# Optimization experiments

Measured on AMD Instinct MI355X. Metric: run time of the kernel, lower is better.

## Reference

```python
import jax, jax.numpy as jnp
import numpy as np
import math

B, S, D = 4, 2048, 768
H = 12
DH = D // H  # 64
NEG = -1e10

def setup_inputs() -> dict:
    key = jax.random.key(0)
    ks = jax.random.split(key, 8)
    scale = 0.02
    return {
        "hidden_states": jax.random.normal(ks[0], (B, S, D), dtype=jnp.float32),
        "attention_mask": jnp.zeros((B, 1, 1, S), dtype=jnp.float32),
        "Wq": jax.random.normal(ks[1], (D, D), dtype=jnp.float32) * scale,
        "bq": jnp.zeros((D,), dtype=jnp.float32),
        "Wk": jax.random.normal(ks[2], (D, D), dtype=jnp.float32) * scale,
        "bk": jnp.zeros((D,), dtype=jnp.float32),
        "Wv": jax.random.normal(ks[3], (D, D), dtype=jnp.float32) * scale,
        "bv": jnp.zeros((D,), dtype=jnp.float32),
    }

def reference(hidden_states, attention_mask, Wq, bq, Wk, bk, Wv, bv):
    # Linear projections; note attention_mask is accepted but unused, matching the torch module.
    def split_heads(x):  # [B,S,D] -> [B,H,S,DH]
        return x.reshape(B, S, H, DH).transpose(0, 2, 1, 3)
    q = split_heads(hidden_states @ Wq + bq)
    k = split_heads(hidden_states @ Wk + bk)
    v = split_heads(hidden_states @ Wv + bv)
    scores = jnp.einsum("bhqd,bhkd->bhqk", q, k) / math.sqrt(DH)
    causal = jnp.tril(jnp.ones((S, S), dtype=bool))  # masked_fill(mask==0, -1e10)
    scores = jnp.where(causal, scores, NEG)
    probs = jax.nn.softmax(scores, axis=-1)
    # dropout prob = 0.0 (eval) -> identity
    ctx = jnp.einsum("bhqk,bhkd->bhqd", probs, v)
    return ctx.transpose(0, 2, 1, 3).reshape(B, S, D)
```

## Files before the change

kernel.cpp:

```cpp
#include <hip/hip_runtime.h>
#include <hip/hip_bf16.h>

#define B_  4
#define S_  2048
#define D_  768
#define H_  12
#define DH_ 64

typedef __bf16 bf16;
typedef __attribute__((ext_vector_type(8))) __bf16 bf16x8;
typedef __attribute__((ext_vector_type(4))) __bf16 bf16x4;
typedef __attribute__((ext_vector_type(4))) float floatx4;
typedef __attribute__((ext_vector_type(16))) float floatx16;

__device__ __forceinline__ void load_lds16(const bf16* g, bf16* l) {
    __builtin_amdgcn_global_load_lds((const __attribute__((address_space(1))) void*)g,
                                     (__attribute__((address_space(3))) void*)l, 16, 0, 0);
}

__device__ __forceinline__ unsigned pack2(float a, float b) {
    unsigned ua = __builtin_bit_cast(unsigned, a) + 0x8000u;
    unsigned ub = __builtin_bit_cast(unsigned, b) + 0x8000u;
    return __builtin_amdgcn_perm(ub, ua, 0x07060302);
}

__device__ __forceinline__ int chunk_off2(int qt2) {
    if (qt2 < 4)  return qt2;
    if (qt2 < 8)  return 4 + 2 * (qt2 - 4);
    if (qt2 < 12) return 12 + 3 * (qt2 - 8);
    return 24 + 4 * (qt2 - 12);
}

__global__ __launch_bounds__(256) void cvt_f32_bf16(const float* __restrict__ in,
                                                    bf16* __restrict__ out, int n4) {
    int i = blockIdx.x * 256 + threadIdx.x;
    if (i < n4) {
        float4 v = ((const float4*)in)[i];
        bf16x4 o;
        o[0] = (bf16)v.x; o[1] = (bf16)v.y; o[2] = (bf16)v.z; o[3] = (bf16)v.w;
        *(bf16x4*)(out + (size_t)i * 4) = o;
    }
}

__global__ __launch_bounds__(256) void w_transpose(const float* __restrict__ w0,
                                                   const float* __restrict__ w1,
                                                   const float* __restrict__ w2,
                                                   bf16* __restrict__ Wt)
{
    const int which = blockIdx.z;
    const float* W = (which == 0) ? w0 : (which == 1 ? w1 : w2);
    bf16* dst = Wt + (size_t)which * D_ * D_;
    __shared__ bf16 t[64 * 72];
    const int k0 = blockIdx.x * 64, n0 = blockIdx.y * 64;
    const int tid = threadIdx.x;
    {
        int r = tid >> 2;
        int c0 = (tid & 3) * 16;
        #pragma unroll
        for (int q = 0; q < 4; q++) {
            float4 v = *(const float4*)(W + (size_t)(k0 + r) * D_ + n0 + c0 + q * 4);
            t[(c0 + q * 4 + 0) * 72 + r] = (bf16)v.x;
            t[(c0 + q * 4 + 1) * 72 + r] = (bf16)v.y;
            t[(c0 + q * 4 + 2) * 72 + r] = (bf16)v.z;
            t[(c0 + q * 4 + 3) * 72 + r] = (bf16)v.w;
        }
    }
    __syncthreads();
    {
        int n = tid >> 3, seg = tid & 7;
        *(bf16x8*)(dst + (size_t)(n0 + n) * D_ + k0 + seg * 8) =
            *(const bf16x8*)(t + n * 72 + seg * 8);
        *(bf16x8*)(dst + (size_t)(n0 + n + 32) * D_ + k0 + seg * 8) =
            *(const bf16x8*)(t + (n + 32) * 72 + seg * 8);
    }
}

__global__ __launch_bounds__(256) void qkv_gemm(
    const bf16* __restrict__ Xb, const bf16* __restrict__ Wt,
    const float* __restrict__ bq, const float* __restrict__ bk,
    const float* __restrict__ bv, bf16* __restrict__ QKV)
{
    const int which = blockIdx.z;
    const bf16* Wm = Wt + (size_t)which * D_ * D_;
    const float* bias = (which == 0) ? bq : (which == 1 ? bk : bv);
    bf16* out = QKV + (size_t)which * B_ * H_ * S_ * DH_;

    __shared__ bf16 As[128 * 64];
    __shared__ bf16 Bs[128 * 64];

    const int tid  = threadIdx.x;
    const int wave = tid >> 6, lane = tid & 63;
    const int wr = wave >> 1, wc = wave & 1;
    const int g = lane >> 4, ln = lane & 15;
    const int m0 = blockIdx.x * 128, n0 = blockIdx.y * 128;
    const int fbase = wave * 256 + lane;

    floatx4 acc[4][4];
    #pragma unroll
    for (int i = 0; i < 4; i++)
        #pragma unroll
        for (int j = 0; j < 4; j++)
            acc[i][j] = (floatx4){0.f, 0.f, 0.f, 0.f};

    for (int k0 = 0; k0 < D_; k0 += 64) {
        __syncthreads();
        #pragma unroll
        for (int i = 0; i < 4; i++) {
            int fc = fbase + i * 64;
            int row = fc >> 3;
            int seg = (fc & 7) ^ (row & 7);
            load_lds16(Xb + (size_t)(m0 + row) * D_ + k0 + seg * 8, As + fc * 8);
            load_lds16(Wm + (size_t)(n0 + row) * D_ + k0 + seg * 8, Bs + fc * 8);
        }
        __syncthreads();
        #pragma unroll
        for (int ks = 0; ks < 2; ks++) {
            const int sx = ((ks * 4 + g) ^ (ln & 7)) * 8;
            bf16x8 af[4], bfr[4];
            #pragma unroll
            for (int i = 0; i < 4; i++)
                af[i] = *(const bf16x8*)(As + ((wr * 64 + i * 16 + ln) << 6) + sx);
            #pragma unroll
            for (int j = 0; j < 4; j++)
                bfr[j] = *(const bf16x8*)(Bs + ((wc * 64 + j * 16 + ln) << 6) + sx);
            #pragma unroll
            for (int i = 0; i < 4; i++)
                #pragma unroll
                for (int j = 0; j < 4; j++)
                    acc[i][j] = __builtin_amdgcn_mfma_f32_16x16x32_bf16(af[i], bfr[j], acc[i][j], 0, 0, 0);
        }
    }

    const float sc = (which == 0) ? 0.125f : 1.0f;
    #pragma unroll
    for (int i = 0; i < 4; i++) {
        #pragma unroll
        for (int j = 0; j < 4; j++) {
            int col = n0 + wc * 64 + j * 16 + ln;
            float bv_ = bias[col];
            int h = col >> 6, dh = col & 63;
            int rowbase = m0 + wr * 64 + i * 16 + g * 4;
            int b = rowbase >> 11, s0 = rowbase & 2047;
            if (which == 2) {
                bf16x4 o;
                #pragma unroll
                for (int r = 0; r < 4; r++) o[r] = (bf16)(acc[i][j][r] + bv_);
                *(bf16x4*)(out + ((size_t)((b * H_ + h) * DH_ + dh)) * S_ + s0) = o;
            } else {
                #pragma unroll
                for (int r = 0; r < 4; r++)
                    out[(((size_t)(b * H_ + h) * S_ + s0 + r) << 6) + dh] =
                        (bf16)((acc[i][j][r] + bv_) * sc);
            }
        }
    }
}

__global__ __launch_bounds__(256, 3) void attn_chunk(const bf16* __restrict__ QKV,
                                                     float* __restrict__ out,
                                                     bf16* __restrict__ Opart,
                                                     float* __restrict__ Lpart)
{
    const int cid = 39 - blockIdx.x;
    const int bh = blockIdx.y;
    const int b = bh / H_, h = bh % H_;

    int qt2, c;
    if (cid < 4)       { qt2 = cid; c = 0; }
    else if (cid < 12) { int t = cid - 4;  qt2 = 4 + (t >> 1);  c = t & 1; }
    else if (cid < 24) { int t = cid - 12; qt2 = 8 + t / 3;     c = t - 3 * (t / 3); }
    else               { int t = cid - 24; qt2 = 12 + (t >> 2); c = t & 3; }
    const int nch = (2 * qt2 + 9) >> 3;
    const int kt0 = c * 8;
    const int kt1 = min(kt0 + 7, 2 * qt2 + 1);

    const size_t MAT = (size_t)B_ * H_ * S_ * DH_;
    const bf16* Q  = QKV +           (size_t)bh * S_ * DH_;
    const bf16* K  = QKV + MAT +     (size_t)bh * S_ * DH_;
    const bf16* Vt = QKV + 2 * MAT + (size_t)bh * S_ * DH_;

    __shared__ bf16 Ks[64 * 72];
    __shared__ bf16 Vts[64 * 72];

    const int tid  = threadIdx.x;
    const int wave = tid >> 6, lane = tid & 63;
    const int l31 = lane & 31, lh = lane >> 5;
    const int srow = tid >> 3, sseg = tid & 7;
    const int qbase = qt2 * 128;
    const int qs = qbase + wave * 32;
    const int q = qs + l31;

    bf16x8 qf[4];
    {
        const bf16* qrow = Q + (size_t)q * DH_ + lh * 8;
        #pragma unroll
        for (int s = 0; s < 4; s++) qf[s] = *(const bf16x8*)(qrow + s * 16);
    }

    floatx16 accO[2];
    #pragma unroll
    for (int dt = 0; dt < 2; dt++)
        #pragma unroll
        for (int e = 0; e < 16; e++) accO[dt][e] = 0.f;
    float lsum[4] = {0.f, 0.f, 0.f, 0.f};

    const bf16* kptr = K  + (size_t)(kt0 * 64 + srow) * DH_ + sseg * 8;
    const bf16* vptr = Vt + (size_t)srow * S_ + kt0 * 64 + sseg * 8;
    bf16x8 ka = *(const bf16x8*)kptr;
    bf16x8 kb = *(const bf16x8*)(kptr + 32 * DH_);
    bf16x8 va = *(const bf16x8*)vptr;
    bf16x8 vb = *(const bf16x8*)(vptr + (size_t)32 * S_);

    for (int kt = kt0; kt <= kt1; ++kt) {
        __syncthreads();
        *(bf16x8*)(Ks  + srow * 72 + sseg * 8) = ka;
        *(bf16x8*)(Ks  + (srow + 32) * 72 + sseg * 8) = kb;
        *(bf16x8*)(Vts + srow * 72 + sseg * 8) = va;
        *(bf16x8*)(Vts + (srow + 32) * 72 + sseg * 8) = vb;
        __syncthreads();
        if (kt < kt1) {
            kptr += 64 * DH_;
            vptr += 64;
            ka = *(const bf16x8*)kptr;
            kb = *(const bf16x8*)(kptr + 32 * DH_);
            va = *(const bf16x8*)vptr;
            vb = *(const bf16x8*)(vptr + (size_t)32 * S_);
        }

        const bool domask = (kt * 64 + 63 > qs);

        #pragma unroll
        for (int kk = 0; kk < 2; kk++) {
            floatx16 accS;
            #pragma unroll
            for (int e = 0; e < 16; e++) accS[e] = 0.f;
            #pragma unroll
            for (int s = 0; s < 4; s++) {
                bf16x8 kf = *(const bf16x8*)(Ks + (kk * 32 + l31) * 72 + s * 16 + lh * 8);
                accS = __builtin_amdgcn_mfma_f32_32x32x16_bf16(kf, qf[s], accS, 0, 0, 0);
            }

            unsigned pk1[4], pk2[4];
            if (domask) {
                const int keyb = kt * 64 + kk * 32 + 4 * lh;
                #pragma unroll
                for (int rq = 0; rq < 4; rq++) {
                    float p[4];
                    #pragma unroll
                    for (int rr = 0; rr < 4; rr++) {
                        float v = __expf(accS[4 * rq + rr]);
                        if (keyb + 8 * rq + rr > q) v = 0.f;
                        p[rr] = v;
                        lsum[rq] += v;
                    }
                    pk1[rq] = pack2(p[0], p[1]);
                    pk2[rq] = pack2(p[2], p[3]);
                }
            } else {
                #pragma unroll
                for (int rq = 0; rq < 4; rq++) {
                    float p[4];
                    #pragma unroll
                    for (int rr = 0; rr < 4; rr++) {
                        float v = __expf(accS[4 * rq + rr]);
                        p[rr] = v;
                        lsum[rq] += v;
                    }
                    pk1[rq] = pack2(p[0], p[1]);
                    pk2[rq] = pack2(p[2], p[3]);
                }
            }

            #pragma unroll
            for (int sl = 0; sl < 2; sl++) {
                const int s = kk * 2 + sl;
                unsigned sendA = lh ? pk1[2 * sl] : pk1[2 * sl + 1];
                unsigned sendB = lh ? pk2[2 * sl] : pk2[2 * sl + 1];
                unsigned recvA = __shfl_xor(sendA, 32, 64);
                unsigned recvB = __shfl_xor(sendB, 32, 64);
                uint4 w;
                w.x = lh ? recvA : pk1[2 * sl];
                w.y = lh ? recvB : pk2[2 * sl];
                w.z = lh ? pk1[2 * sl + 1] : recvA;
                w.w = lh ? pk2[2 * sl + 1] : recvB;
                bf16x8 ptf = __builtin_bit_cast(bf16x8, w);
                #pragma unroll
                for (int dt = 0; dt < 2; dt++) {
                    bf16x8 vf = *(const bf16x8*)(Vts + (dt * 32 + l31) * 72 + s * 16 + lh * 8);
                    accO[dt] = __builtin_amdgcn_mfma_f32_32x32x16_bf16(vf, ptf, accO[dt], 0, 0, 0);
                }
            }
        }
    }

    const float Lr = (lsum[0] + lsum[1]) + (lsum[2] + lsum[3]);
    const float L = Lr + __shfl_xor(Lr, 32, 64);

    if (nch == 1) {
        const float inv = 1.0f / L;
        float* orow = out + (size_t)(b * S_ + q) * D_ + h * DH_;
        #pragma unroll
        for (int dt = 0; dt < 2; dt++)
            #pragma unroll
            for (int rq = 0; rq < 4; rq++) {
                float4 o;
                o.x = accO[dt][4 * rq + 0] * inv; o.y = accO[dt][4 * rq + 1] * inv;
                o.z = accO[dt][4 * rq + 2] * inv; o.w = accO[dt][4 * rq + 3] * inv;
                *(float4*)(orow + dt * 32 + 8 * rq + 4 * lh) = o;
            }
    } else {
        const int chunk = bh * 40 + chunk_off2(qt2) + c;
        bf16* obase = Opart + (size_t)chunk * 8192 + (wave * 32 + l31) * 64;
        #pragma unroll
        for (int dt = 0; dt < 2; dt++)
            #pragma unroll
            for (int rq = 0; rq < 4; rq++) {
                bf16x4 o;
                #pragma unroll
                for (int rr = 0; rr < 4; rr++) o[rr] = (bf16)accO[dt][4 * rq + rr];
                *(bf16x4*)(obase + dt * 32 + 8 * rq + 4 * lh) = o;
            }
        if (lh == 0) Lpart[chunk * 128 + wave * 32 + l31] = L;
    }
}

__global__ __launch_bounds__(256) void attn_reduce(const bf16* __restrict__ Opart,
                                                   const float* __restrict__ Lpart,
                                                   float* __restrict__ out)
{
    const int qt2 = 4 + blockIdx.x;
    const int bh = blockIdx.y;
    const int b = bh / H_, h = bh % H_;
    const int nch = (2 * qt2 + 9) >> 3;
    const int cb = bh * 40 + chunk_off2(qt2);

    const int e = threadIdx.x;
    const int ql = e >> 1, dh0 = (e & 1) * 32;

    float o[32];
    #pragma unroll
    for (int i = 0; i < 32; i++) o[i] = 0.f;
    float l = 0.f;

    for (int cidx = 0; cidx < nch; cidx++) {
        const bf16* p = Opart + (size_t)(cb + cidx) * 8192 + ql * 64 + dh0;
        #pragma unroll
        for (int m = 0; m < 4; m++) {
            bf16x8 v = *(const bf16x8*)(p + m * 8);
            #pragma unroll
            for (int k = 0; k < 8; k++) o[m * 8 + k] += (float)v[k];
        }
        l += Lpart[(cb + cidx) * 128 + ql];
    }
    float inv = 1.0f / l;
    float* orow = out + (size_t)(b * S_ + qt2 * 128 + ql) * D_ + h * DH_ + dh0;
    #pragma unroll
    for (int m = 0; m < 8; m++) {
        float4 v;
        v.x = o[m * 4 + 0] * inv; v.y = o[m * 4 + 1] * inv;
        v.z = o[m * 4 + 2] * inv; v.w = o[m * 4 + 3] * inv;
        *(float4*)(orow + m * 4) = v;
    }
}

extern "C" void kernel_launch(void* const* d_in, const int* in_sizes, int n_in,
                              void* d_out, int out_size, void* d_ws, size_t ws_size,
                              hipStream_t stream) {
    const float* hs = (const float*)d_in[0];
    const float* Wq = (const float*)d_in[2];
    const float* bq = (const float*)d_in[3];
    const float* Wk = (const float*)d_in[4];
    const float* bk = (const float*)d_in[5];
    const float* Wv = (const float*)d_in[6];
    const float* bv = (const float*)d_in[7];
    float* out = (float*)d_out;

    bf16* Xb    = (bf16*)d_ws;
    bf16* Wt    = Xb + (size_t)8192 * 768;
    bf16* QKV   = Wt + (size_t)3 * 768 * 768;
    bf16* Opart = QKV + (size_t)3 * B_ * H_ * S_ * DH_;
    float* Lpart = (float*)(Opart + (size_t)1920 * 8192);

    cvt_f32_bf16<<<6144, 256, 0, stream>>>(hs, Xb, 1572864);
    w_transpose<<<dim3(12, 12, 3), 256, 0, stream>>>(Wq, Wk, Wv, Wt);
    qkv_gemm<<<dim3(64, 6, 3), 256, 0, stream>>>(Xb, Wt, bq, bk, bv, QKV);
    attn_chunk<<<dim3(40, 48), 256, 0, stream>>>(QKV, out, Opart, Lpart);
    attn_reduce<<<dim3(12, 48), 256, 0, stream>>>(Opart, Lpart, out);
}
```

Before: 202.9 us.

## Double-buffer LDS with direct global-to-LDS loads in GEMM and attention; use 32x32 MFMA

```diff
diff --git a/kernel.cpp b/kernel.cpp
--- a/kernel.cpp
+++ b/kernel.cpp
@@ -85,81 +85,105 @@
     const float* bias = (which == 0) ? bq : (which == 1 ? bk : bv);
     bf16* out = QKV + (size_t)which * B_ * H_ * S_ * DH_;
 
-    __shared__ bf16 As[128 * 64];
-    __shared__ bf16 Bs[128 * 64];
+    __shared__ bf16 As[2][128 * 64];
+    __shared__ bf16 Bs[2][128 * 64];
 
     const int tid  = threadIdx.x;
     const int wave = tid >> 6, lane = tid & 63;
     const int wr = wave >> 1, wc = wave & 1;
-    const int g = lane >> 4, ln = lane & 15;
+    const int l31 = lane & 31, lh = lane >> 5;
     const int m0 = blockIdx.x * 128, n0 = blockIdx.y * 128;
-    const int fbase = wave * 256 + lane;
-
-    floatx4 acc[4][4];
-    #pragma unroll
-    for (int i = 0; i < 4; i++)
-        #pragma unroll
-        for (int j = 0; j < 4; j++)
-            acc[i][j] = (floatx4){0.f, 0.f, 0.f, 0.f};
-
-    for (int k0 = 0; k0 < D_; k0 += 64) {
+
+    int row_[4], off_[4], lds_[4];
+    #pragma unroll
+    for (int i = 0; i < 4; i++) {
+        int fc = i * 256 + tid;
+        int row = fc >> 3;
+        row_[i] = row;
+        off_[i] = ((fc & 7) ^ (row & 7)) * 8;
+        lds_[i] = fc * 8;
+    }
+
+    floatx16 acc[2][2];
+    #pragma unroll
+    for (int mt = 0; mt < 2; mt++)
+        #pragma unroll
+        for (int nt = 0; nt < 2; nt++)
+            #pragma unroll
+            for (int e = 0; e < 16; e++) acc[mt][nt][e] = 0.f;
+
+    #pragma unroll
+    for (int i = 0; i < 4; i++) {
+        load_lds16(Xb + (size_t)(m0 + row_[i]) * D_ + off_[i], &As[0][lds_[i]]);
+        load_lds16(Wm + (size_t)(n0 + row_[i]) * D_ + off_[i], &Bs[0][lds_[i]]);
+    }
+
+    const int rxor = l31 & 7;
+    for (int it = 0; it < 12; ++it) {
+        const int cur = it & 1;
         __syncthreads();
-        #pragma unroll
-        for (int i = 0; i < 4; i++) {
-            int fc = fbase + i * 64;
-            int row = fc >> 3;
-            int seg = (fc & 7) ^ (row & 7);
-            load_lds16(Xb + (size_t)(m0 + row) * D_ + k0 + seg * 8, As + fc * 8);
-            load_lds16(Wm + (size_t)(n0 + row) * D_ + k0 + seg * 8, Bs + fc * 8);
-        }
-        __syncthreads();
-        #pragma unroll
-        for (int ks = 0; ks < 2; ks++) {
-            const int sx = ((ks * 4 + g) ^ (ln & 7)) * 8;
-            bf16x8 af[4], bfr[4];
-            #pragma unroll
-            for (int i = 0; i < 4; i++)
-                af[i] = *(const bf16x8*)(As + ((wr * 64 + i * 16 + ln) << 6) + sx);
-            #pragma unroll
-            for (int j = 0; j < 4; j++)
-                bfr[j] = *(const bf16x8*)(Bs + ((wc * 64 + j * 16 + ln) << 6) + sx);
-            #pragma unroll
-            for (int i = 0; i < 4; i++)
+        if (it + 1 < 12) {
+            const int kn = (it + 1) * 64;
+            #pragma unroll
+            for (int i = 0; i < 4; i++) {
+                load_lds16(Xb + (size_t)(m0 + row_[i]) * D_ + kn + off_[i], &As[cur ^ 1][lds_[i]]);
+                load_lds16(Wm + (size_t)(n0 + row_[i]) * D_ + kn + off_[i], &Bs[cur ^ 1][lds_[i]]);
+            }
+        }
+        const bf16* Ac = As[cur];
+        const bf16* Bc = Bs[cur];
+        #pragma unroll
+        for (int s = 0; s < 4; s++) {
+            const int sx = (((s << 1) | lh) ^ rxor) << 3;
+            bf16x8 af[2], bfr[2];
+            #pragma unroll
+            for (int mt = 0; mt < 2; mt++)
+                af[mt] = *(const bf16x8*)(Ac + ((wr * 64 + mt * 32 + l31) << 6) + sx);
+            #pragma unroll
+            for (int nt = 0; nt < 2; nt++)
+                bfr[nt] = *(const bf16x8*)(Bc + ((wc * 64 + nt * 32 + l31) << 6) + sx);
+            #pragma unroll
+            for (int mt = 0; mt < 2; mt++)
                 #pragma unroll
-                for (int j = 0; j < 4; j++)
-                    acc[i][j] = __builtin_amdgcn_mfma_f32_16x16x32_bf16(af[i], bfr[j], acc[i][j], 0, 0, 0);
+                for (int nt = 0; nt < 2; nt++)
+                    acc[mt][nt] = __builtin_amdgcn_mfma_f32_32x32x16_bf16(
+                        af[mt], bfr[nt], acc[mt][nt], 0, 0, 0);
         }
     }
 
     const float sc = (which == 0) ? 0.125f : 1.0f;
     #pragma unroll
-    for (int i = 0; i < 4; i++) {
-        #pragma unroll
-        for (int j = 0; j < 4; j++) {
-            int col = n0 + wc * 64 + j * 16 + ln;
-            float bv_ = bias[col];
-            int h = col >> 6, dh = col & 63;
-            int rowbase = m0 + wr * 64 + i * 16 + g * 4;
-            int b = rowbase >> 11, s0 = rowbase & 2047;
-            if (which == 2) {
-                bf16x4 o;
-                #pragma unroll
-                for (int r = 0; r < 4; r++) o[r] = (bf16)(acc[i][j][r] + bv_);
-                *(bf16x4*)(out + ((size_t)((b * H_ + h) * DH_ + dh)) * S_ + s0) = o;
-            } else {
-                #pragma unroll
-                for (int r = 0; r < 4; r++)
-                    out[(((size_t)(b * H_ + h) * S_ + s0 + r) << 6) + dh] =
-                        (bf16)((acc[i][j][r] + bv_) * sc);
-            }
-        }
-    }
-}
-
-__global__ __launch_bounds__(256, 3) void attn_chunk(const bf16* __restrict__ QKV,
-                                                     float* __restrict__ out,
-                                                     bf16* __restrict__ Opart,
-                                                     float* __restrict__ Lpart)
+    for (int mt = 0; mt < 2; mt++) {
+        #pragma unroll
+        for (int nt = 0; nt < 2; nt++) {
+            const int n = n0 + wc * 64 + nt * 32 + l31;
+            const float bv_ = bias[n];
+            const int h = n >> 6, dh = n & 63;
+            const int mb = m0 + wr * 64 + mt * 32 + 4 * lh;
+            #pragma unroll
+            for (int rq = 0; rq < 4; rq++) {
+                const int m = mb + 8 * rq;
+                const int b = m >> 11, s0 = m & 2047;
+                if (which == 2) {
+                    bf16x4 o;
+                    #pragma unroll
+                    for (int rr = 0; rr < 4; rr++) o[rr] = (bf16)(acc[mt][nt][4 * rq + rr] + bv_);
+                    *(bf16x4*)(out + ((size_t)((b * H_ + h) * DH_ + dh)) * S_ + s0) = o;
+                } else {
+                    #pragma unroll
+                    for (int rr = 0; rr < 4; rr++)
+                        out[(((size_t)(b * H_ + h) * S_ + s0 + rr) << 6) + dh] =
+                            (bf16)((acc[mt][nt][4 * rq + rr] + bv_) * sc);
+                }
+            }
+        }
+    }
+}
+
+__global__ __launch_bounds__(256) void attn_chunk(const bf16* __restrict__ QKV,
+                                                  float* __restrict__ out,
+                                                  bf16* __restrict__ Opart,
+                                                  float* __restrict__ Lpart)
 {
     const int cid = 39 - blockIdx.x;
     const int bh = blockIdx.y;
@@ -179,17 +203,26 @@
     const bf16* K  = QKV + MAT +     (size_t)bh * S_ * DH_;
     const bf16* Vt = QKV + 2 * MAT + (size_t)bh * S_ * DH_;
 
-    __shared__ bf16 Ks[64 * 72];
-    __shared__ bf16 Vts[64 * 72];
+    __shared__ bf16 Ks[2][64 * 64];
+    __shared__ bf16 Vs[2][64 * 64];
 
     const int tid  = threadIdx.x;
     const int wave = tid >> 6, lane = tid & 63;
     const int l31 = lane & 31, lh = lane >> 5;
-    const int srow = tid >> 3, sseg = tid & 7;
     const int qbase = qt2 * 128;
     const int qs = qbase + wave * 32;
     const int q = qs + l31;
 
+    int srow_[2], soff_[2], slds_[2];
+    #pragma unroll
+    for (int i = 0; i < 2; i++) {
+        int fc = i * 256 + tid;
+        int row = fc >> 3;
+        srow_[i] = row;
+        soff_[i] = ((fc & 7) ^ (row & 7)) * 8;
+        slds_[i] = fc * 8;
+    }
+
     bf16x8 qf[4];
     {
         const bf16* qrow = Q + (size_t)q * DH_ + lh * 8;
@@ -204,28 +237,27 @@
         for (int e = 0; e < 16; e++) accO[dt][e] = 0.f;
     float lsum[4] = {0.f, 0.f, 0.f, 0.f};
 
-    const bf16* kptr = K  + (size_t)(kt0 * 64 + srow) * DH_ + sseg * 8;
-    const bf16* vptr = Vt + (size_t)srow * S_ + kt0 * 64 + sseg * 8;
-    bf16x8 ka = *(const bf16x8*)kptr;
-    bf16x8 kb = *(const bf16x8*)(kptr + 32 * DH_);
-    bf16x8 va = *(const bf16x8*)vptr;
-    bf16x8 vb = *(const bf16x8*)(vptr + (size_t)32 * S_);
-
+    #pragma unroll
+    for (int i = 0; i < 2; i++) {
+        load_lds16(K + ((size_t)(kt0 * 64 + srow_[i]) << 6) + soff_[i], &Ks[0][slds_[i]]);
+        load_lds16(Vt + (size_t)srow_[i] * S_ + kt0 * 64 + soff_[i], &Vs[0][slds_[i]]);
+    }
+
+    const int rxor = l31 & 7;
     for (int kt = kt0; kt <= kt1; ++kt) {
-        __syncthreads();
-        *(bf16x8*)(Ks  + srow * 72 + sseg * 8) = ka;
-        *(bf16x8*)(Ks  + (srow + 32) * 72 + sseg * 8) = kb;
-        *(bf16x8*)(Vts + srow * 72 + sseg * 8) = va;
-        *(bf16x8*)(Vts + (srow + 32) * 72 + sseg * 8) = vb;
+        const int cur = (kt - kt0) & 1;
         __syncthreads();
         if (kt < kt1) {
-            kptr += 64 * DH_;
-            vptr += 64;
-            ka = *(const bf16x8*)kptr;
-            kb = *(const bf16x8*)(kptr + 32 * DH_);
-            va = *(const bf16x8*)vptr;
-            vb = *(const bf16x8*)(vptr + (size_t)32 * S_);
-        }
+            #pragma unroll
+            for (int i = 0; i < 2; i++) {
+                load_lds16(K + ((size_t)((kt + 1) * 64 + srow_[i]) << 6) + soff_[i],
+                           &Ks[cur ^ 1][slds_[i]]);
+                load_lds16(Vt + (size_t)srow_[i] * S_ + (kt + 1) * 64 + soff_[i],
+                           &Vs[cur ^ 1][slds_[i]]);
+            }
+        }
+        const bf16* Kc = Ks[cur];
+        const bf16* Vc = Vs[cur];
 
         const bool domask = (kt * 64 + 63 > qs);
 
@@ -236,7 +268,8 @@
             for (int e = 0; e < 16; e++) accS[e] = 0.f;
             #pragma unroll
             for (int s = 0; s < 4; s++) {
-                bf16x8 kf = *(const bf16x8*)(Ks + (kk * 32 + l31) * 72 + s * 16 + lh * 8);
+                const int sx = (((s << 1) | lh) ^ rxor) << 3;
+                bf16x8 kf = *(const bf16x8*)(Kc + ((kk * 32 + l31) << 6) + sx);
                 accS = __builtin_amdgcn_mfma_f32_32x32x16_bf16(kf, qf[s], accS, 0, 0, 0);
             }
 
@@ -284,9 +317,10 @@
                 w.z = lh ? pk1[2 * sl + 1] : recvA;
                 w.w = lh ? pk2[2 * sl + 1] : recvB;
                 bf16x8 ptf = __builtin_bit_cast(bf16x8, w);
+                const int sx = (((s << 1) | lh) ^ rxor) << 3;
                 #pragma unroll
                 for (int dt = 0; dt < 2; dt++) {
-                    bf16x8 vf = *(const bf16x8*)(Vts + (dt * 32 + l31) * 72 + s * 16 + lh * 8);
+                    bf16x8 vf = *(const bf16x8*)(Vc + ((dt * 32 + l31) << 6) + sx);
                     accO[dt] = __builtin_amdgcn_mfma_f32_32x32x16_bf16(vf, ptf, accO[dt], 0, 0, 0);
                 }
             }
```

After: 206.6 us. About the same (+1.8%).
